# Kernel optimization log

Hardware: AMD Instinct MI355X
Metric: run time of the kernel (lower is better)

The kernel has to match this reference:

```python
import jax, jax.numpy as jnp
import numpy as np

N, CS, CZ = 512, 384, 128
H, C, PQ, PV = 12, 16, 4, 8
NB = 8
EPS = 1e-8


def _ln(x, g, b):
    m = jnp.mean(x, axis=-1, keepdims=True)
    v = jnp.mean((x - m) ** 2, axis=-1, keepdims=True)
    return (x - m) / jnp.sqrt(v + 1e-5) * g + b


def _quat_rot(bcd):
    # (1, b, c, d) quaternion -> rotation matrix, as in AF2 BackboneUpdate
    ones = jnp.ones(bcd.shape[:-1] + (1,), bcd.dtype)
    q = jnp.concatenate([ones, bcd], axis=-1)
    q = q / jnp.linalg.norm(q, axis=-1, keepdims=True)
    w, x, y, z = q[..., 0], q[..., 1], q[..., 2], q[..., 3]
    R = jnp.stack([
        1 - 2 * (y * y + z * z), 2 * (x * y - w * z), 2 * (x * z + w * y),
        2 * (x * y + w * z), 1 - 2 * (x * x + z * z), 2 * (y * z - w * x),
        2 * (x * z - w * y), 2 * (y * z + w * x), 1 - 2 * (x * x + y * y),
    ], axis=-1)
    return R.reshape(bcd.shape[:-1] + (3, 3))


def _ipa(s, z, R, t, p):
    n = s.shape[0]
    q = (s @ p['w_q']).reshape(n, H, C)
    kv = (s @ p['w_kv']).reshape(n, H, 2, C)
    k, v = kv[..., 0, :], kv[..., 1, :]

    # local points -> global frames
    q_pts = (s @ p['w_qpts']).reshape(n, H * PQ, 3)
    q_pts = jnp.einsum('nxy,npy->npx', R, q_pts) + t[:, None, :]
    q_pts = q_pts.reshape(n, H, PQ, 3)
    kv_pts = (s @ p['w_kvpts']).reshape(n, H * (PQ + PV), 3)
    kv_pts = jnp.einsum('nxy,npy->npx', R, kv_pts) + t[:, None, :]
    kv_pts = kv_pts.reshape(n, H, PQ + PV, 3)
    k_pts, v_pts = kv_pts[:, :, :PQ], kv_pts[:, :, PQ:]

    b = z @ p['w_b']  # [i, j, H]

    scalar = jnp.einsum('ihc,jhc->hij', q, k) / np.sqrt(C)
    # sum_p ||q_ip - k_jp||^2 expanded to avoid [N,N,H,P,3] intermediate
    sq_q = jnp.sum(q_pts ** 2, axis=(-1, -2)).T  # [H, i]
    sq_k = jnp.sum(k_pts ** 2, axis=(-1, -2)).T  # [H, j]
    cross = jnp.einsum('ihpc,jhpc->hij', q_pts, k_pts)
    d2 = sq_q[:, :, None] + sq_k[:, None, :] - 2.0 * cross  # [H, i, j]

    gamma = jax.nn.softplus(p['head_weights'])  # [H]
    w_C = np.sqrt(2.0 / (9.0 * PQ))
    w_L = np.sqrt(1.0 / 3.0)
    logits = w_L * (scalar + jnp.transpose(b, (2, 0, 1))
                    - gamma[:, None, None] * (w_C / 2.0) * d2)
    a = jax.nn.softmax(logits, axis=-1)  # [H, i, j]

    o = jnp.einsum('hij,jhc->ihc', a, v).reshape(n, H * C)
    o_pt = jnp.einsum('hij,jhpc->ihpc', a, v_pts)
    # back to local frame: R_i^{-1} (o_pt - t_i)
    o_pt = jnp.einsum('nyx,nhpy->nhpx', R, o_pt - t[:, None, None, :])
    o_pt_norm = jnp.sqrt(jnp.sum(o_pt ** 2, axis=-1) + EPS)  # [n, H, PV]
    o_pair = jnp.einsum('hij,ijz->ihz', a, z).reshape(n, H * CZ)

    cat = jnp.concatenate([o, o_pt.reshape(n, H * PV * 3),
                           o_pt_norm.reshape(n, H * PV), o_pair], axis=-1)
    return cat @ p['w_out'] + p['b_out']


def _forward(s, z, p):
    n = s.shape[0]
    R = jnp.broadcast_to(jnp.eye(3, dtype=s.dtype), (n, 3, 3))
    t = jnp.zeros((n, 3), s.dtype)
    for _ in range(NB):  # shared weights across blocks, as in AF2
        s = s + _ipa(s, z, R, t, p)
        s = _ln(s, p['ln1_g'], p['ln1_b'])
        h = jax.nn.relu(s @ p['w_t1'])
        h = jax.nn.relu(h @ p['w_t2'])
        s = s + h @ p['w_t3']
        s = _ln(s, p['ln2_g'], p['ln2_b'])
        upd = s @ p['w_bb'] + p['b_bb']  # [n, 6]
        Ru = _quat_rot(upd[:, :3])
        tu = upd[:, 3:]
        t = jnp.einsum('nxy,ny->nx', R, tu) + t
        R = jnp.einsum('nxy,nyz->nxz', R, Ru)
    return jnp.concatenate([s, t], axis=-1)  # [n, CS + 3]


def setup_inputs() -> dict:
    key = jax.random.key(0)
    ks = jax.random.split(key, 12)
    sc = 0.02
    cat_dim = H * C + H * PV * 3 + H * PV + H * CZ  # 2112
    return {
        's': jax.random.normal(ks[0], (N, CS), jnp.float32),
        'z': jax.random.normal(ks[1], (N, N, CZ), jnp.float32),
        'w_q': jax.random.normal(ks[2], (CS, H * C), jnp.float32) * sc,
        'w_kv': jax.random.normal(ks[3], (CS, H * 2 * C), jnp.float32) * sc,
        'w_qpts': jax.random.normal(ks[4], (CS, H * PQ * 3), jnp.float32) * sc,
        'w_kvpts': jax.random.normal(ks[5], (CS, H * (PQ + PV) * 3), jnp.float32) * sc,
        'w_b': jax.random.normal(ks[6], (CZ, H), jnp.float32) * sc,
        'head_weights': jnp.zeros((H,), jnp.float32),
        'w_out': jax.random.normal(ks[7], (cat_dim, CS), jnp.float32) * sc,
        'b_out': jnp.zeros((CS,), jnp.float32),
        'ln1_g': jnp.ones((CS,), jnp.float32),
        'ln1_b': jnp.zeros((CS,), jnp.float32),
        'w_t1': jax.random.normal(ks[8], (CS, CS), jnp.float32) * sc,
        'w_t2': jax.random.normal(ks[9], (CS, CS), jnp.float32) * sc,
        'w_t3': jax.random.normal(ks[10], (CS, CS), jnp.float32) * sc,
        'ln2_g': jnp.ones((CS,), jnp.float32),
        'ln2_b': jnp.zeros((CS,), jnp.float32),
        'w_bb': jax.random.normal(ks[11], (CS, 6), jnp.float32) * sc,
        'b_bb': jnp.zeros((6,), jnp.float32),
    }


def reference(s, z, w_q, w_kv, w_qpts, w_kvpts, w_b, head_weights, w_out,
              b_out, ln1_g, ln1_b, w_t1, w_t2, w_t3, ln2_g, ln2_b, w_bb, b_bb):
    p = dict(w_q=w_q, w_kv=w_kv, w_qpts=w_qpts, w_kvpts=w_kvpts, w_b=w_b,
             head_weights=head_weights, w_out=w_out, b_out=b_out,
             ln1_g=ln1_g, ln1_b=ln1_b, w_t1=w_t1, w_t2=w_t2, w_t3=w_t3,
             ln2_g=ln2_g, ln2_b=ln2_b, w_bb=w_bb, b_bb=b_bb)
    return _forward(s, z, p)
```

## Files before the change

kernel.cpp:

```cpp
#include <hip/hip_runtime.h>
#include <hip/hip_bf16.h>

constexpr int Nres = 512;
constexpr int Cs   = 384;
constexpr int Cz   = 128;
constexpr int NH   = 12;
constexpr int HC   = 16;
constexpr int NPQ  = 4;
constexpr int NPV  = 8;
constexpr int NBLK = 8;
constexpr int PROJD = NH*HC + NH*2*HC + NH*NPQ*3 + NH*(NPQ+NPV)*3;
constexpr int CATD = NH*HC + NH*NPV*3 + NH*NPV + NH*Cz;
constexpr float W_L  = 0.57735026918962576f;
constexpr float W_C2 = 0.11785113019775793f;

using u16 = unsigned short;
typedef __bf16 bf16x8 __attribute__((ext_vector_type(8)));
typedef float  f32x4  __attribute__((ext_vector_type(4)));

static inline int gdiv(int n, int b) { return (n + b - 1) / b; }

static __device__ __forceinline__ u16 f2bf(float x) {
    __hip_bfloat16 h = __float2bfloat16(x);
    return *reinterpret_cast<u16*>(&h);
}
static __device__ __forceinline__ float bf2f(u16 x) {
    return __bfloat162float(*reinterpret_cast<__hip_bfloat16*>(&x));
}

__global__ void k_init(const float* __restrict__ s_in, float* __restrict__ s_cur,
                       u16* __restrict__ s_bf,
                       float* __restrict__ R, float* __restrict__ t) {
    int idx = blockIdx.x * blockDim.x + threadIdx.x;
    if (idx < Nres * Cs) { float v = s_in[idx]; s_cur[idx] = v; s_bf[idx] = f2bf(v); }
    if (idx < Nres * 9) {
        int e = idx % 9;
        R[idx] = (e == 0 || e == 4 || e == 8) ? 1.f : 0.f;
    }
    if (idx < Nres * 3) t[idx] = 0.f;
}

__global__ void k_concatW(const float* __restrict__ w_q, const float* __restrict__ w_kv,
                          const float* __restrict__ w_qpts, const float* __restrict__ w_kvpts,
                          float* __restrict__ Wcat) {
    int idx = blockIdx.x * blockDim.x + threadIdx.x;
    if (idx >= Cs * PROJD) return;
    int k = idx / PROJD, n = idx - k * PROJD;
    float v;
    if      (n < 192) v = w_q[k * 192 + n];
    else if (n < 576) v = w_kv[k * 384 + (n - 192)];
    else if (n < 720) v = w_qpts[k * 144 + (n - 576)];
    else              v = w_kvpts[k * 432 + (n - 720)];
    Wcat[idx] = v;
}

__global__ void k_transposeW(const float* __restrict__ in, u16* __restrict__ out,
                             int K, int N) {
    __shared__ float tile[32][33];
    int n0 = blockIdx.x * 32, k0 = blockIdx.y * 32;
    int tx = threadIdx.x & 31, ty = threadIdx.x >> 5;
#pragma unroll
    for (int j = 0; j < 4; j++)
        tile[ty + j * 8][tx] = in[(size_t)(k0 + ty + j * 8) * N + n0 + tx];
    __syncthreads();
#pragma unroll
    for (int j = 0; j < 4; j++)
        out[(size_t)(n0 + ty + j * 8) * K + k0 + tx] = f2bf(tile[tx][ty + j * 8]);
}

__global__ void k_zT(const float* __restrict__ z, u16* __restrict__ zT) {
    __shared__ float tile[32][33];
    int i  = blockIdx.x;
    int j0 = blockIdx.y * 32;
    int c0 = blockIdx.z * 32;
    int tx = threadIdx.x & 31, ty = threadIdx.x >> 5;
    const float* src = z + (size_t)i * Nres * Cz;
#pragma unroll
    for (int l = 0; l < 4; l++)
        tile[ty + l * 8][tx] = src[(size_t)(j0 + ty + l * 8) * Cz + c0 + tx];
    __syncthreads();
    u16* dst = zT + (size_t)i * Cz * Nres;
#pragma unroll
    for (int l = 0; l < 4; l++)
        dst[(size_t)(c0 + ty + l * 8) * Nres + j0 + tx] = f2bf(tile[tx][ty + l * 8]);
}

__global__ void __launch_bounds__(256)
k_gemm_mfma(const u16* __restrict__ A, const u16* __restrict__ Bt,
            float* __restrict__ P, int M, int K, int N, int Kc) {
    __shared__ u16 As[2][64 * 40];
    __shared__ u16 Bs[2][64 * 40];
    const int tid = threadIdx.x;
    const int m0 = blockIdx.y * 64;
    const int n0 = blockIdx.x * 64;
    const int kbeg = blockIdx.z * Kc;
    const int kend = kbeg + Kc;
    const int wv = tid >> 6, lane = tid & 63;
    const int wm = (wv >> 1) * 32, wn = (wv & 1) * 32;
    const int lrow = lane & 15, lq = lane >> 4;

    f32x4 zero = {0.f, 0.f, 0.f, 0.f};
    f32x4 acc00 = zero, acc01 = zero, acc10 = zero, acc11 = zero;

    const int srow = tid >> 2;
    const int sko  = (tid & 3) * 8;
    const size_t aoff = (size_t)(m0 + srow) * K + sko;
    const size_t boff = (size_t)(n0 + srow) * K + sko;

    uint4 ra = *(const uint4*)&A[aoff + kbeg];
    uint4 rb = *(const uint4*)&Bt[boff + kbeg];
    *(uint4*)&As[0][srow * 40 + sko] = ra;
    *(uint4*)&Bs[0][srow * 40 + sko] = rb;
    __syncthreads();

    int buf = 0;
    for (int k0 = kbeg; k0 < kend; k0 += 32) {
        const bool nxt = (k0 + 32 < kend);
        if (nxt) {
            ra = *(const uint4*)&A[aoff + k0 + 32];
            rb = *(const uint4*)&Bt[boff + k0 + 32];
        }
        bf16x8 a0 = *reinterpret_cast<const bf16x8*>(&As[buf][(wm + lrow) * 40 + lq * 8]);
        bf16x8 a1 = *reinterpret_cast<const bf16x8*>(&As[buf][(wm + 16 + lrow) * 40 + lq * 8]);
        bf16x8 b0 = *reinterpret_cast<const bf16x8*>(&Bs[buf][(wn + lrow) * 40 + lq * 8]);
        bf16x8 b1 = *reinterpret_cast<const bf16x8*>(&Bs[buf][(wn + 16 + lrow) * 40 + lq * 8]);
        acc00 = __builtin_amdgcn_mfma_f32_16x16x32_bf16(a0, b0, acc00, 0, 0, 0);
        acc01 = __builtin_amdgcn_mfma_f32_16x16x32_bf16(a0, b1, acc01, 0, 0, 0);
        acc10 = __builtin_amdgcn_mfma_f32_16x16x32_bf16(a1, b0, acc10, 0, 0, 0);
        acc11 = __builtin_amdgcn_mfma_f32_16x16x32_bf16(a1, b1, acc11, 0, 0, 0);
        if (nxt) {
            *(uint4*)&As[buf ^ 1][srow * 40 + sko] = ra;
            *(uint4*)&Bs[buf ^ 1][srow * 40 + sko] = rb;
            __syncthreads();
            buf ^= 1;
        }
    }
    float* Pp = P + (size_t)blockIdx.z * M * N;
    const int rbase = m0 + wm + lq * 4;
    const int cbase = n0 + wn + lrow;
#pragma unroll
    for (int r = 0; r < 4; r++) {
        Pp[(size_t)(rbase + r) * N + cbase]           = acc00[r];
        Pp[(size_t)(rbase + r) * N + cbase + 16]      = acc01[r];
        Pp[(size_t)(rbase + 16 + r) * N + cbase]      = acc10[r];
        Pp[(size_t)(rbase + 16 + r) * N + cbase + 16] = acc11[r];
    }
}

__global__ void __launch_bounds__(256)
k_gemm_rbf(const u16* __restrict__ A, const u16* __restrict__ Bt,
           float* __restrict__ outf, u16* __restrict__ outb,
           int M, int K, int N, int relu_bf) {
    __shared__ u16 As[2][32 * 40];
    __shared__ u16 Bs[2][64 * 40];
    const int tid = threadIdx.x;
    const int m0 = blockIdx.y * 32;
    const int n0 = blockIdx.x * 64;
    const int wv = tid >> 6, lane = tid & 63;
    const int wm = (wv >> 1) * 16, wn = (wv & 1) * 32;
    const int lrow = lane & 15, lq = lane >> 4;
    f32x4 zero = {0.f, 0.f, 0.f, 0.f};
    f32x4 acc0 = zero, acc1 = zero;
    const int srow = tid >> 2, sko = (tid & 3) * 8;
    const size_t aoff = (size_t)(m0 + srow) * K + sko;
    const size_t boff = (size_t)(n0 + srow) * K + sko;

    uint4 ra, rb;
    if (tid < 128) ra = *(const uint4*)&A[aoff];
    rb = *(const uint4*)&Bt[boff];
    if (tid < 128) *(uint4*)&As[0][srow * 40 + sko] = ra;
    *(uint4*)&Bs[0][srow * 40 + sko] = rb;
    __syncthreads();

    int buf = 0;
    for (int k0 = 0; k0 < K; k0 += 32) {
        const bool nxt = (k0 + 32 < K);
        if (nxt) {
            if (tid < 128) ra = *(const uint4*)&A[aoff + k0 + 32];
            rb = *(const uint4*)&Bt[boff + k0 + 32];
        }
        bf16x8 a  = *reinterpret_cast<const bf16x8*>(&As[buf][(wm + lrow) * 40 + lq * 8]);
        bf16x8 b0 = *reinterpret_cast<const bf16x8*>(&Bs[buf][(wn + lrow) * 40 + lq * 8]);
        bf16x8 b1 = *reinterpret_cast<const bf16x8*>(&Bs[buf][(wn + 16 + lrow) * 40 + lq * 8]);
        acc0 = __builtin_amdgcn_mfma_f32_16x16x32_bf16(a, b0, acc0, 0, 0, 0);
        acc1 = __builtin_amdgcn_mfma_f32_16x16x32_bf16(a, b1, acc1, 0, 0, 0);
        if (nxt) {
            if (tid < 128) *(uint4*)&As[buf ^ 1][srow * 40 + sko] = ra;
            *(uint4*)&Bs[buf ^ 1][srow * 40 + sko] = rb;
            __syncthreads();
            buf ^= 1;
        }
    }
    const int rbase = m0 + wm + lq * 4;
    const int cbase = n0 + wn + lrow;
    if (relu_bf) {
#pragma unroll
        for (int r = 0; r < 4; r++) {
            outb[(size_t)(rbase + r) * N + cbase]      = f2bf(fmaxf(acc0[r], 0.f));
            outb[(size_t)(rbase + r) * N + cbase + 16] = f2bf(fmaxf(acc1[r], 0.f));
        }
    } else {
#pragma unroll
        for (int r = 0; r < 4; r++) {
            outf[(size_t)(rbase + r) * N + cbase]      = acc0[r];
            outf[(size_t)(rbase + r) * N + cbase + 16] = acc1[r];
        }
    }
}

__global__ void k_bproj(const float* __restrict__ z, const float* __restrict__ w_b,
                        float* __restrict__ b_hij) {
    __shared__ float zs[16][129];
    __shared__ float wbs[Cz * NH];
    const int tid = threadIdx.x;
    const int base = blockIdx.x * 16;
#pragma unroll
    for (int l = 0; l < 6; l++) {
        int idx = tid + l * 256;
        if (idx < Cz * NH) wbs[idx] = w_b[idx];
    }
#pragma unroll
    for (int l = 0; l < 8; l++) {
        int idx = tid + l * 256;
        int r = idx >> 7, c = idx & 127;
        zs[r][c] = z[(size_t)(base + r) * Cz + c];
    }
    __syncthreads();
    if (tid < 192) {
        int h = tid >> 4, r = tid & 15;
        float acc = 0.f;
        for (int c = 0; c < Cz; c++) acc += zs[r][c] * wbs[c * NH + h];
        int row = base + r;
        int i = row >> 9, j = row & 511;
        b_hij[((size_t)h * Nres + i) * Nres + j] = acc * W_L;
    }
}

__global__ void k_prep(const float* __restrict__ proj, const float* __restrict__ R,
                       const float* __restrict__ t, const float* __restrict__ hw,
                       u16* __restrict__ Aaug, u16* __restrict__ Baug,
                       u16* __restrict__ vhT) {
    int idx = blockIdx.x * blockDim.x + threadIdx.x;
    if (idx >= NH * Nres) return;
    int h = idx / Nres, i = idx % Nres;
    float R_[9], t_[3];
#pragma unroll
    for (int e = 0; e < 9; e++) R_[e] = R[i * 9 + e];
#pragma unroll
    for (int e = 0; e < 3; e++) t_[e] = t[i * 3 + e];
    const float* prow = proj + (size_t)i * PROJD;
    float gam = log1pf(__expf(hw[h]));
    float ch  = sqrtf(2.f * gam * W_C2);

    u16 arow[32], brow[32];
#pragma unroll
    for (int c = 0; c < HC; c++) {
        arow[c] = f2bf(prow[h * HC + c] * (W_L * 0.25f));
        brow[c] = f2bf(prow[192 + h * 2 * HC + c]);
        vhT[((size_t)h * 48 + c) * Nres + i] = f2bf(prow[192 + h * 2 * HC + HC + c]);
    }
#pragma unroll
    for (int p = 0; p < NPQ; p++) {
        const float* src = prow + 576 + (h * NPQ + p) * 3;
        float y0 = src[0], y1 = src[1], y2 = src[2];
        float v0 = R_[0]*y0 + R_[1]*y1 + R_[2]*y2 + t_[0];
        float v1 = R_[3]*y0 + R_[4]*y1 + R_[5]*y2 + t_[1];
        float v2 = R_[6]*y0 + R_[7]*y1 + R_[8]*y2 + t_[2];
        float s = W_L * ch;
        arow[16 + p*3 + 0] = f2bf(v0 * s);
        arow[16 + p*3 + 1] = f2bf(v1 * s);
        arow[16 + p*3 + 2] = f2bf(v2 * s);
    }
    float sk = 0.f;
#pragma unroll
    for (int p = 0; p < NPQ + NPV; p++) {
        const float* src = prow + 720 + (h * (NPQ+NPV) + p) * 3;
        float y0 = src[0], y1 = src[1], y2 = src[2];
        float v0 = R_[0]*y0 + R_[1]*y1 + R_[2]*y2 + t_[0];
        float v1 = R_[3]*y0 + R_[4]*y1 + R_[5]*y2 + t_[1];
        float v2 = R_[6]*y0 + R_[7]*y1 + R_[8]*y2 + t_[2];
        if (p < NPQ) {
            brow[16 + p*3 + 0] = f2bf(v0 * ch);
            brow[16 + p*3 + 1] = f2bf(v1 * ch);
            brow[16 + p*3 + 2] = f2bf(v2 * ch);
            sk += v0*v0 + v1*v1 + v2*v2;
        } else {
            int c0 = 16 + (p - NPQ) * 3;
            vhT[((size_t)h * 48 + c0 + 0) * Nres + i] = f2bf(v0);
            vhT[((size_t)h * 48 + c0 + 1) * Nres + i] = f2bf(v1);
            vhT[((size_t)h * 48 + c0 + 2) * Nres + i] = f2bf(v2);
        }
    }
    float x = -W_L * gam * W_C2 * sk;
    u16 hi = f2bf(x);
    float lo = x - bf2f(hi);
    arow[28] = f2bf(1.0f); arow[29] = f2bf(1.0f); arow[30] = 0; arow[31] = 0;
    brow[28] = hi;         brow[29] = f2bf(lo);   brow[30] = 0; brow[31] = 0;

    uint4* ad = (uint4*)&Aaug[((size_t)h * Nres + i) * 32];
    uint4* bd = (uint4*)&Baug[((size_t)h * Nres + i) * 32];
    const uint4* as = (const uint4*)arow;
    const uint4* bs = (const uint4*)brow;
#pragma unroll
    for (int e = 0; e < 4; e++) { ad[e] = as[e]; bd[e] = bs[e]; }
}

__global__ void __launch_bounds__(256)
k_attn(const u16* __restrict__ Aaug, const u16* __restrict__ Baug,
       const float* __restrict__ b_hij, const u16* __restrict__ vhT,
       const float* __restrict__ R, const float* __restrict__ t,
       u16* __restrict__ Pbf, u16* __restrict__ cat_bf) {
    __shared__ union {
        struct { u16 A[64 * 40]; u16 B[512 * 40]; } qk;
        u16 P[64 * 520];
    } U;
    __shared__ u16 Bsv[2][48 * 40];
    __shared__ float Ct[64 * 49];

    const int i0 = blockIdx.x * 64;
    const int h  = blockIdx.y;
    const int tid = threadIdx.x;
    const int wv = tid >> 6, lane = tid & 63;
    const int lrow = lane & 15, lq = lane >> 4;
    const int wm = wv * 16;
    const int srow = tid >> 2, sko = (tid & 3) * 8;

    const u16* Bp = vhT + (size_t)h * 48 * Nres;
    const size_t boff = (size_t)srow * Nres + sko;
    if (tid < 192) {
        uint4 rv = *(const uint4*)&Bp[boff];
        *(uint4*)&Bsv[0][srow * 40 + sko] = rv;
    }

    {
        int r4 = tid >> 2, q = tid & 3;
        *(uint4*)&U.qk.A[r4 * 40 + q * 8] =
            *(const uint4*)&Aaug[((size_t)h * Nres + i0 + r4) * 32 + q * 8];
#pragma unroll
        for (int l = 0; l < 8; l++) {
            int idx = tid + l * 256;
            int rr = idx >> 2, qq = idx & 3;
            *(uint4*)&U.qk.B[rr * 40 + qq * 8] =
                *(const uint4*)&Baug[((size_t)h * Nres + rr) * 32 + qq * 8];
        }
    }
    __syncthreads();

    f32x4 zero = {0.f, 0.f, 0.f, 0.f};
    bf16x8 afrag = *reinterpret_cast<const bf16x8*>(&U.qk.A[(wm + lrow) * 40 + lq * 8]);
    f32x4 acc[32];
#pragma unroll
    for (int tt = 0; tt < 32; tt++) {
        bf16x8 bfr = *reinterpret_cast<const bf16x8*>(&U.qk.B[(tt * 16 + lrow) * 40 + lq * 8]);
        acc[tt] = __builtin_amdgcn_mfma_f32_16x16x32_bf16(afrag, bfr, zero, 0, 0, 0);
    }
    const float* bh = b_hij + ((size_t)h * Nres + (i0 + wm + lq * 4)) * Nres;
#pragma unroll
    for (int tt = 0; tt < 32; tt++) {
#pragma unroll
        for (int r = 0; r < 4; r++)
            acc[tt][r] += bh[(size_t)r * Nres + tt * 16 + lrow];
    }
    float mx[4] = {-1e30f, -1e30f, -1e30f, -1e30f};
#pragma unroll
    for (int tt = 0; tt < 32; tt++)
#pragma unroll
        for (int r = 0; r < 4; r++) mx[r] = fmaxf(mx[r], acc[tt][r]);
#pragma unroll
    for (int off = 8; off > 0; off >>= 1)
#pragma unroll
        for (int r = 0; r < 4; r++) mx[r] = fmaxf(mx[r], __shfl_xor(mx[r], off));
    float sm[4] = {0.f, 0.f, 0.f, 0.f};
#pragma unroll
    for (int tt = 0; tt < 32; tt++)
#pragma unroll
        for (int r = 0; r < 4; r++) { acc[tt][r] = __expf(acc[tt][r] - mx[r]); sm[r] += acc[tt][r]; }
#pragma unroll
    for (int off = 8; off > 0; off >>= 1)
#pragma unroll
        for (int r = 0; r < 4; r++) sm[r] += __shfl_xor(sm[r], off);
    float inv[4];
#pragma unroll
    for (int r = 0; r < 4; r++) inv[r] = 1.f / sm[r];

    __syncthreads();

#pragma unroll
    for (int tt = 0; tt < 32; tt++)
#pragma unroll
        for (int r = 0; r < 4; r++)
            U.P[(wm + lq * 4 + r) * 520 + tt * 16 + lrow] = f2bf(acc[tt][r] * inv[r]);
    __syncthreads();

#pragma unroll
    for (int l = 0; l < 16; l++) {
        int v = tid + l * 256;
        int rr = v >> 6, cq = v & 63;
        *(uint4*)&Pbf[((size_t)h * Nres + i0 + rr) * 512 + cq * 8] =
            *(const uint4*)&U.P[rr * 520 + cq * 8];
    }

    f32x4 o0 = zero, o1 = zero, o2 = zero;
    int buf = 0;
    for (int k0 = 0; k0 < Nres; k0 += 32) {
        const bool nxt = (k0 + 32 < Nres);
        uint4 rv;
        if (nxt && tid < 192) rv = *(const uint4*)&Bp[boff + k0 + 32];
        bf16x8 a  = *reinterpret_cast<const bf16x8*>(&U.P[(wm + lrow) * 520 + k0 + lq * 8]);
        bf16x8 b0 = *reinterpret_cast<const bf16x8*>(&Bsv[buf][(lrow) * 40 + lq * 8]);
        bf16x8 b1 = *reinterpret_cast<const bf16x8*>(&Bsv[buf][(16 + lrow) * 40 + lq * 8]);
        bf16x8 b2 = *reinterpret_cast<const bf16x8*>(&Bsv[buf][(32 + lrow) * 40 + lq * 8]);
        o0 = __builtin_amdgcn_mfma_f32_16x16x32_bf16(a, b0, o0, 0, 0, 0);
        o1 = __builtin_amdgcn_mfma_f32_16x16x32_bf16(a, b1, o1, 0, 0, 0);
        o2 = __builtin_amdgcn_mfma_f32_16x16x32_bf16(a, b2, o2, 0, 0, 0);
        if (nxt) {
            if (tid < 192) *(uint4*)&Bsv[buf ^ 1][srow * 40 + sko] = rv;
            __syncthreads();
            buf ^= 1;
        }
    }
#pragma unroll
    for (int r = 0; r < 4; r++) {
        int row = wm + lq * 4 + r;
        Ct[row * 49 + lrow]      = o0[r];
        Ct[row * 49 + 16 + lrow] = o1[r];
        Ct[row * 49 + 32 + lrow] = o2[r];
    }
    __syncthreads();
#pragma unroll
    for (int l = 0; l < 4; l++) {
        int idx = tid + l * 256;
        int r = idx >> 4, c = idx & 15;
        cat_bf[(size_t)(i0 + r) * CATD + h * HC + c] = f2bf(Ct[r * 49 + c]);
    }
#pragma unroll
    for (int l = 0; l < 2; l++) {
        int idx = tid + l * 256;
        int r = idx >> 3, p = idx & 7;
        int i = i0 + r;
        float g0 = Ct[r * 49 + 16 + p * 3 + 0];
        float g1 = Ct[r * 49 + 16 + p * 3 + 1];
        float g2 = Ct[r * 49 + 16 + p * 3 + 2];
        float d0 = g0 - t[i * 3 + 0], d1 = g1 - t[i * 3 + 1], d2v = g2 - t[i * 3 + 2];
        const float* Rn = R + i * 9;
        float l0 = Rn[0] * d0 + Rn[3] * d1 + Rn[6] * d2v;
        float l1 = Rn[1] * d0 + Rn[4] * d1 + Rn[7] * d2v;
        float l2 = Rn[2] * d0 + Rn[5] * d1 + Rn[8] * d2v;
        int hp = h * NPV + p;
        u16* crow = cat_bf + (size_t)i * CATD;
        crow[192 + hp * 3 + 0] = f2bf(l0);
        crow[192 + hp * 3 + 1] = f2bf(l1);
        crow[192 + hp * 3 + 2] = f2bf(l2);
        crow[480 + hp] = f2bf(sqrtf(l0 * l0 + l1 * l1 + l2 * l2 + 1e-8f));
    }
}

__global__ void __launch_bounds__(256)
k_opair(const u16* __restrict__ Pbf, const u16* __restrict__ zT,
        u16* __restrict__ cat_bf) {
    __shared__ u16 P_lds[16 * 520];
    __shared__ u16 Bs[2][128 * 40];
    const int i = blockIdx.x;
    const int tid = threadIdx.x;
    const int wv = tid >> 6, ln = tid & 63;
    const int srow = tid >> 2, sko = (tid & 3) * 8;
    const u16* Bp = zT + (size_t)i * Cz * Nres;
    const size_t b0off = (size_t)srow * Nres + sko;
    const size_t b1off = (size_t)(64 + srow) * Nres + sko;

    uint4 rb0 = *(const uint4*)&Bp[b0off];
    uint4 rb1 = *(const uint4*)&Bp[b1off];

#pragma unroll
    for (int l = 0; l < 3; l++) {
        int v = tid + l * 256;
        int hh = v >> 6, cq = v & 63;
        *(uint4*)&P_lds[hh * 520 + cq * 8] =
            *(const uint4*)&Pbf[((size_t)hh * Nres + i) * 512 + cq * 8];
    }
    for (int l = tid; l < 4 * 520; l += 256) P_lds[12 * 520 + l] = 0;

    *(uint4*)&Bs[0][srow * 40 + sko]        = rb0;
    *(uint4*)&Bs[0][(64 + srow) * 40 + sko] = rb1;
    __syncthreads();

    const int lrow = ln & 15, lq = ln >> 4;
    const int wn = wv * 32;
    f32x4 zero = {0.f, 0.f, 0.f, 0.f};
    f32x4 acc0 = zero, acc1 = zero;
    int buf = 0;
    for (int k0 = 0; k0 < Nres; k0 += 32) {
        const bool nxt = (k0 + 32 < Nres);
        if (nxt) {
            rb0 = *(const uint4*)&Bp[b0off + k0 + 32];
            rb1 = *(const uint4*)&Bp[b1off + k0 + 32];
        }
        bf16x8 a  = *reinterpret_cast<const bf16x8*>(&P_lds[lrow * 520 + k0 + lq * 8]);
        bf16x8 b0 = *reinterpret_cast<const bf16x8*>(&Bs[buf][(wn + lrow) * 40 + lq * 8]);
        bf16x8 b1 = *reinterpret_cast<const bf16x8*>(&Bs[buf][(wn + 16 + lrow) * 40 + lq * 8]);
        acc0 = __builtin_amdgcn_mfma_f32_16x16x32_bf16(a, b0, acc0, 0, 0, 0);
        acc1 = __builtin_amdgcn_mfma_f32_16x16x32_bf16(a, b1, acc1, 0, 0, 0);
        if (nxt) {
            *(uint4*)&Bs[buf ^ 1][srow * 40 + sko]        = rb0;
            *(uint4*)&Bs[buf ^ 1][(64 + srow) * 40 + sko] = rb1;
            __syncthreads();
            buf ^= 1;
        }
    }
    u16* crow = cat_bf + (size_t)i * CATD + 576;
#pragma unroll
    for (int r = 0; r < 4; r++) {
        int row = lq * 4 + r;
        if (row < NH) {
            crow[row * Cz + wn + lrow]      = f2bf(acc0[r]);
            crow[row * Cz + wn + 16 + lrow] = f2bf(acc1[r]);
        }
    }
}

__global__ void k_reduce_ln(const float* __restrict__ P, const float* __restrict__ bias,
                            float* __restrict__ s, u16* __restrict__ s_bf,
                            const float* __restrict__ g, const float* __restrict__ b,
                            int nsplit) {
    __shared__ float red[512];
    int i = blockIdx.x, tid = threadIdx.x;
    float v = s[(size_t)i * Cs + tid];
    if (bias) v += bias[tid];
    for (int sp = 0; sp < nsplit; sp++) v += P[(size_t)sp * Nres * Cs + (size_t)i * Cs + tid];
    red[tid] = v;
    if (tid < 128) red[384 + tid] = 0.f;
    __syncthreads();
    for (int st = 256; st > 0; st >>= 1) { if (tid < st) red[tid] += red[tid + st]; __syncthreads(); }
    float mean = red[0] / Cs;
    __syncthreads();
    float d = v - mean;
    red[tid] = d * d;
    if (tid < 128) red[384 + tid] = 0.f;
    __syncthreads();
    for (int st = 256; st > 0; st >>= 1) { if (tid < st) red[tid] += red[tid + st]; __syncthreads(); }
    float var = red[0] / Cs;
    float o = d * rsqrtf(var + 1e-5f) * g[tid] + b[tid];
    s[(size_t)i * Cs + tid] = o;
    s_bf[(size_t)i * Cs + tid] = f2bf(o);
}

__global__ void k_reduce_ln_bb(const float* __restrict__ P, float* __restrict__ s,
                               u16* __restrict__ s_bf,
                               const float* __restrict__ g, const float* __restrict__ b,
                               int nsplit,
                               const float* __restrict__ w_bb, const float* __restrict__ b_bb,
                               float* __restrict__ R, float* __restrict__ t) {
    __shared__ float red[512];
    __shared__ float uw[36];
    int i = blockIdx.x, tid = threadIdx.x;
    float v = s[(size_t)i * Cs + tid];
    for (int sp = 0; sp < nsplit; sp++) v += P[(size_t)sp * Nres * Cs + (size_t)i * Cs + tid];
    red[tid] = v;
    if (tid < 128) red[384 + tid] = 0.f;
    __syncthreads();
    for (int st = 256; st > 0; st >>= 1) { if (tid < st) red[tid] += red[tid + st]; __syncthreads(); }
    float mean = red[0] / Cs;
    __syncthreads();
    float d = v - mean;
    red[tid] = d * d;
    if (tid < 128) red[384 + tid] = 0.f;
    __syncthreads();
    for (int st = 256; st > 0; st >>= 1) { if (tid < st) red[tid] += red[tid + st]; __syncthreads(); }
    float var = red[0] / Cs;
    float o = d * rsqrtf(var + 1e-5f) * g[tid] + b[tid];
    s[(size_t)i * Cs + tid] = o;
    s_bf[(size_t)i * Cs + tid] = f2bf(o);

    float u[6];
#pragma unroll
    for (int dd = 0; dd < 6; dd++) u[dd] = o * w_bb[tid * 6 + dd];
#pragma unroll
    for (int off = 32; off > 0; off >>= 1)
#pragma unroll
        for (int dd = 0; dd < 6; dd++) u[dd] += __shfl_xor(u[dd], off);
    int wv = tid >> 6, lane = tid & 63;
    if (lane == 0) {
#pragma unroll
        for (int dd = 0; dd < 6; dd++) uw[wv * 6 + dd] = u[dd];
    }
    __syncthreads();
    if (tid == 0) {
        float uu[6];
#pragma unroll
        for (int dd = 0; dd < 6; dd++) {
            float a = b_bb[dd];
            for (int w = 0; w < 6; w++) a += uw[w * 6 + dd];
            uu[dd] = a;
        }
        float qb = uu[0], qc = uu[1], qd = uu[2];
        float inv = rsqrtf(1.f + qb*qb + qc*qc + qd*qd);
        float w = inv, x = qb * inv, y = qc * inv, zq = qd * inv;
        float Ru[9] = {
            1.f - 2.f*(y*y + zq*zq), 2.f*(x*y - w*zq),       2.f*(x*zq + w*y),
            2.f*(x*y + w*zq),        1.f - 2.f*(x*x + zq*zq), 2.f*(y*zq - w*x),
            2.f*(x*zq - w*y),        2.f*(y*zq + w*x),        1.f - 2.f*(x*x + y*y)
        };
        float Ro[9];
#pragma unroll
        for (int e = 0; e < 9; e++) Ro[e] = R[i * 9 + e];
        float tu0 = uu[3], tu1 = uu[4], tu2 = uu[5];
        t[i*3+0] += Ro[0]*tu0 + Ro[1]*tu1 + Ro[2]*tu2;
        t[i*3+1] += Ro[3]*tu0 + Ro[4]*tu1 + Ro[5]*tu2;
        t[i*3+2] += Ro[6]*tu0 + Ro[7]*tu1 + Ro[8]*tu2;
#pragma unroll
        for (int r = 0; r < 3; r++)
#pragma unroll
            for (int c = 0; c < 3; c++)
                R[i*9 + r*3 + c] = Ro[r*3+0]*Ru[0*3+c] + Ro[r*3+1]*Ru[1*3+c] + Ro[r*3+2]*Ru[2*3+c];
    }
}

__global__ void k_final(const float* __restrict__ s, const float* __restrict__ t,
                        float* __restrict__ out) {
    int idx = blockIdx.x * blockDim.x + threadIdx.x;
    if (idx >= Nres * (Cs + 3)) return;
    int i = idx / (Cs + 3), c = idx - i * (Cs + 3);
    out[idx] = (c < Cs) ? s[(size_t)i * Cs + c] : t[i * 3 + (c - Cs)];
}

extern "C" void kernel_launch(void* const* d_in, const int* in_sizes, int n_in,
                              void* d_out, int out_size, void* d_ws, size_t ws_size,
                              hipStream_t stream) {
    const float* s_in    = (const float*)d_in[0];
    const float* z       = (const float*)d_in[1];
    const float* w_q     = (const float*)d_in[2];
    const float* w_kv    = (const float*)d_in[3];
    const float* w_qpts  = (const float*)d_in[4];
    const float* w_kvpts = (const float*)d_in[5];
    const float* w_b     = (const float*)d_in[6];
    const float* hw      = (const float*)d_in[7];
    const float* w_out   = (const float*)d_in[8];
    const float* b_out   = (const float*)d_in[9];
    const float* ln1_g   = (const float*)d_in[10];
    const float* ln1_b   = (const float*)d_in[11];
    const float* w_t1    = (const float*)d_in[12];
    const float* w_t2    = (const float*)d_in[13];
    const float* w_t3    = (const float*)d_in[14];
    const float* ln2_g   = (const float*)d_in[15];
    const float* ln2_b   = (const float*)d_in[16];
    const float* w_bb    = (const float*)d_in[17];
    const float* b_bb    = (const float*)d_in[18];
    float* out = (float*)d_out;

    float* ws = (float*)d_ws;
    size_t off = 0;
    float* s_cur = ws + off; off += (size_t)Nres * Cs;
    float* b_hij = ws + off; off += (size_t)NH * Nres * Nres;
    float* proj  = ws + off; off += (size_t)Nres * PROJD;
    float* Wcat  = ws + off; off += (size_t)Cs * PROJD;
    float* Rbuf  = ws + off; off += (size_t)Nres * 9;
    float* tbuf  = ws + off; off += (size_t)Nres * 3;
    float* Pslab = ws + off; off += (size_t)11 * Nres * Cs;
    u16* s_bf   = (u16*)(ws + off); off += (size_t)Nres * Cs / 2;
    u16* cat_bf = (u16*)(ws + off); off += (size_t)Nres * CATD / 2;
    u16* h1_bf  = (u16*)(ws + off); off += (size_t)Nres * Cs / 2;
    u16* h2_bf  = (u16*)(ws + off); off += (size_t)Nres * Cs / 2;
    u16* WcatT  = (u16*)(ws + off); off += (size_t)Cs * PROJD / 2;
    u16* w_outT = (u16*)(ws + off); off += (size_t)CATD * Cs / 2;
    u16* w_t1T  = (u16*)(ws + off); off += (size_t)Cs * Cs / 2;
    u16* w_t2T  = (u16*)(ws + off); off += (size_t)Cs * Cs / 2;
    u16* w_t3T  = (u16*)(ws + off); off += (size_t)Cs * Cs / 2;
    u16* Pbf    = (u16*)(ws + off); off += (size_t)NH * Nres * Nres / 2;
    u16* vhTbf  = (u16*)(ws + off); off += (size_t)NH * 48 * Nres / 2;
    u16* Aaug   = (u16*)(ws + off); off += (size_t)NH * Nres * 32 / 2;
    u16* Baug   = (u16*)(ws + off); off += (size_t)NH * Nres * 32 / 2;
    u16* zTbf   = (u16*)(ws + off); off += (size_t)Nres * Cz * Nres / 2;

    k_init<<<gdiv(Nres*Cs, 256), 256, 0, stream>>>(s_in, s_cur, s_bf, Rbuf, tbuf);
    k_concatW<<<gdiv(Cs*PROJD, 256), 256, 0, stream>>>(w_q, w_kv, w_qpts, w_kvpts, Wcat);
    k_transposeW<<<dim3(PROJD/32, Cs/32), 256, 0, stream>>>(Wcat, WcatT, Cs, PROJD);
    k_transposeW<<<dim3(Cs/32, CATD/32), 256, 0, stream>>>(w_out, w_outT, CATD, Cs);
    k_transposeW<<<dim3(Cs/32, Cs/32), 256, 0, stream>>>(w_t1, w_t1T, Cs, Cs);
    k_transposeW<<<dim3(Cs/32, Cs/32), 256, 0, stream>>>(w_t2, w_t2T, Cs, Cs);
    k_transposeW<<<dim3(Cs/32, Cs/32), 256, 0, stream>>>(w_t3, w_t3T, Cs, Cs);
    k_bproj<<<Nres*Nres/16, 256, 0, stream>>>(z, w_b, b_hij);
    k_zT<<<dim3(Nres, Nres/32, Cz/32), 256, 0, stream>>>(z, zTbf);

    for (int it = 0; it < NBLK; it++) {
        k_gemm_rbf<<<dim3(PROJD/64, Nres/32), 256, 0, stream>>>(s_bf, WcatT, proj, nullptr, Nres, Cs, PROJD, 0);
        k_prep<<<gdiv(NH*Nres, 256), 256, 0, stream>>>(proj, Rbuf, tbuf, hw, Aaug, Baug, vhTbf);
        k_attn<<<dim3(Nres/64, NH), 256, 0, stream>>>(Aaug, Baug, b_hij, vhTbf, Rbuf, tbuf, Pbf, cat_bf);
        k_opair<<<Nres, 256, 0, stream>>>(Pbf, zTbf, cat_bf);
        k_gemm_mfma<<<dim3(Cs/64, Nres/64, 6), 256, 0, stream>>>(cat_bf, w_outT, Pslab, Nres, CATD, Cs, 352);
        k_reduce_ln<<<Nres, Cs, 0, stream>>>(Pslab, b_out, s_cur, s_bf, ln1_g, ln1_b, 6);
        k_gemm_rbf<<<dim3(Cs/64, Nres/32), 256, 0, stream>>>(s_bf, w_t1T, nullptr, h1_bf, Nres, Cs, Cs, 1);
        k_gemm_rbf<<<dim3(Cs/64, Nres/32), 256, 0, stream>>>(h1_bf, w_t2T, nullptr, h2_bf, Nres, Cs, Cs, 1);
        k_gemm_rbf<<<dim3(Cs/64, Nres/32), 256, 0, stream>>>(h2_bf, w_t3T, Pslab, nullptr, Nres, Cs, Cs, 0);
        k_reduce_ln_bb<<<Nres, Cs, 0, stream>>>(Pslab, s_cur, s_bf, ln2_g, ln2_b, 1, w_bb, b_bb, Rbuf, tbuf);
    }

    k_final<<<gdiv(Nres*(Cs+3), 256), 256, 0, stream>>>(s_cur, tbuf, out);
}
```

Measured before the change: 919.5 us.

## Store pair bias in bf16, transpose proj output, split-K transition GEMMs

```diff
diff --git a/kernel.cpp b/kernel.cpp
--- a/kernel.cpp
+++ b/kernel.cpp
@@ -148,9 +148,8 @@
 }
 
 __global__ void __launch_bounds__(256)
-k_gemm_rbf(const u16* __restrict__ A, const u16* __restrict__ Bt,
-           float* __restrict__ outf, u16* __restrict__ outb,
-           int M, int K, int N, int relu_bf) {
+k_gemm_proj(const u16* __restrict__ A, const u16* __restrict__ Bt,
+            float* __restrict__ outT, int M, int K, int N) {
     __shared__ u16 As[2][32 * 40];
     __shared__ u16 Bs[2][64 * 40];
     const int tid = threadIdx.x;
@@ -193,23 +192,86 @@
     }
     const int rbase = m0 + wm + lq * 4;
     const int cbase = n0 + wn + lrow;
-    if (relu_bf) {
-#pragma unroll
-        for (int r = 0; r < 4; r++) {
-            outb[(size_t)(rbase + r) * N + cbase]      = f2bf(fmaxf(acc0[r], 0.f));
-            outb[(size_t)(rbase + r) * N + cbase + 16] = f2bf(fmaxf(acc1[r], 0.f));
-        }
-    } else {
-#pragma unroll
-        for (int r = 0; r < 4; r++) {
-            outf[(size_t)(rbase + r) * N + cbase]      = acc0[r];
-            outf[(size_t)(rbase + r) * N + cbase + 16] = acc1[r];
-        }
+    *reinterpret_cast<f32x4*>(&outT[(size_t)cbase * M + rbase])        = acc0;
+    *reinterpret_cast<f32x4*>(&outT[(size_t)(cbase + 16) * M + rbase]) = acc1;
+}
+
+__global__ void __launch_bounds__(256)
+k_gemm_tr(const u16* __restrict__ Abf, const float* __restrict__ As0,
+          const float* __restrict__ As1, const u16* __restrict__ Bt,
+          float* __restrict__ Pout, int amode) {
+    __shared__ u16 Asm[2][32 * 40];
+    __shared__ u16 Bsm[2][64 * 40];
+    const int tid = threadIdx.x;
+    const int m0 = blockIdx.y * 32;
+    const int n0 = blockIdx.x * 64;
+    const int kbeg = blockIdx.z * 192;
+    const int kend = kbeg + 192;
+    const int wv = tid >> 6, lane = tid & 63;
+    const int wm = (wv >> 1) * 16, wn = (wv & 1) * 32;
+    const int lrow = lane & 15, lq = lane >> 4;
+    f32x4 zero = {0.f, 0.f, 0.f, 0.f};
+    f32x4 acc0 = zero, acc1 = zero;
+    const int srow = tid >> 2, sko = (tid & 3) * 8;
+    const int rowR = tid >> 3, c4 = (tid & 7) * 4;
+    const size_t aoffb = (size_t)(m0 + srow) * Cs + sko;
+    const size_t aoffr = (size_t)(m0 + rowR) * Cs + c4;
+    const size_t boff  = (size_t)(n0 + srow) * Cs + sko;
+
+    uint4 ra, rb;
+    float4 f0, f1;
+    rb = *(const uint4*)&Bt[boff + kbeg];
+    if (amode == 0) { if (tid < 128) ra = *(const uint4*)&Abf[aoffb + kbeg]; }
+    else { f0 = *(const float4*)&As0[aoffr + kbeg]; f1 = *(const float4*)&As1[aoffr + kbeg]; }
+
+    if (amode == 0) { if (tid < 128) *(uint4*)&Asm[0][srow * 40 + sko] = ra; }
+    else {
+        uint2 wp;
+        wp.x = (unsigned)f2bf(fmaxf(f0.x + f1.x, 0.f)) | ((unsigned)f2bf(fmaxf(f0.y + f1.y, 0.f)) << 16);
+        wp.y = (unsigned)f2bf(fmaxf(f0.z + f1.z, 0.f)) | ((unsigned)f2bf(fmaxf(f0.w + f1.w, 0.f)) << 16);
+        *(uint2*)&Asm[0][rowR * 40 + c4] = wp;
+    }
+    *(uint4*)&Bsm[0][srow * 40 + sko] = rb;
+    __syncthreads();
+
+    int buf = 0;
+    for (int k0 = kbeg; k0 < kend; k0 += 32) {
+        const bool nxt = (k0 + 32 < kend);
+        if (nxt) {
+            rb = *(const uint4*)&Bt[boff + k0 + 32];
+            if (amode == 0) { if (tid < 128) ra = *(const uint4*)&Abf[aoffb + k0 + 32]; }
+            else { f0 = *(const float4*)&As0[aoffr + k0 + 32]; f1 = *(const float4*)&As1[aoffr + k0 + 32]; }
+        }
+        bf16x8 a  = *reinterpret_cast<const bf16x8*>(&Asm[buf][(wm + lrow) * 40 + lq * 8]);
+        bf16x8 b0 = *reinterpret_cast<const bf16x8*>(&Bsm[buf][(wn + lrow) * 40 + lq * 8]);
+        bf16x8 b1 = *reinterpret_cast<const bf16x8*>(&Bsm[buf][(wn + 16 + lrow) * 40 + lq * 8]);
+        acc0 = __builtin_amdgcn_mfma_f32_16x16x32_bf16(a, b0, acc0, 0, 0, 0);
+        acc1 = __builtin_amdgcn_mfma_f32_16x16x32_bf16(a, b1, acc1, 0, 0, 0);
+        if (nxt) {
+            if (amode == 0) { if (tid < 128) *(uint4*)&Asm[buf ^ 1][srow * 40 + sko] = ra; }
+            else {
+                uint2 wp;
+                wp.x = (unsigned)f2bf(fmaxf(f0.x + f1.x, 0.f)) | ((unsigned)f2bf(fmaxf(f0.y + f1.y, 0.f)) << 16);
+                wp.y = (unsigned)f2bf(fmaxf(f0.z + f1.z, 0.f)) | ((unsigned)f2bf(fmaxf(f0.w + f1.w, 0.f)) << 16);
+                *(uint2*)&Asm[buf ^ 1][rowR * 40 + c4] = wp;
+            }
+            *(uint4*)&Bsm[buf ^ 1][srow * 40 + sko] = rb;
+            __syncthreads();
+            buf ^= 1;
+        }
+    }
+    float* Pp = Pout + (size_t)blockIdx.z * Nres * Cs;
+    const int rbase = m0 + wm + lq * 4;
+    const int cbase = n0 + wn + lrow;
+#pragma unroll
+    for (int r = 0; r < 4; r++) {
+        Pp[(size_t)(rbase + r) * Cs + cbase]      = acc0[r];
+        Pp[(size_t)(rbase + r) * Cs + cbase + 16] = acc1[r];
     }
 }
 
 __global__ void k_bproj(const float* __restrict__ z, const float* __restrict__ w_b,
-                        float* __restrict__ b_hij) {
+                        u16* __restrict__ b_hij_bf) {
     __shared__ float zs[16][129];
     __shared__ float wbs[Cz * NH];
     const int tid = threadIdx.x;
@@ -232,37 +294,37 @@
         for (int c = 0; c < Cz; c++) acc += zs[r][c] * wbs[c * NH + h];
         int row = base + r;
         int i = row >> 9, j = row & 511;
-        b_hij[((size_t)h * Nres + i) * Nres + j] = acc * W_L;
-    }
-}
-
-__global__ void k_prep(const float* __restrict__ proj, const float* __restrict__ R,
+        b_hij_bf[((size_t)h * Nres + i) * Nres + j] = f2bf(acc * W_L);
+    }
+}
+
+__global__ void k_prep(const float* __restrict__ projT, const float* __restrict__ R,
                        const float* __restrict__ t, const float* __restrict__ hw,
                        u16* __restrict__ Aaug, u16* __restrict__ Baug,
                        u16* __restrict__ vhT) {
     int idx = blockIdx.x * blockDim.x + threadIdx.x;
     if (idx >= NH * Nres) return;
     int h = idx / Nres, i = idx % Nres;
+#define PR(col) projT[(size_t)(col) * Nres + i]
     float R_[9], t_[3];
 #pragma unroll
     for (int e = 0; e < 9; e++) R_[e] = R[i * 9 + e];
 #pragma unroll
     for (int e = 0; e < 3; e++) t_[e] = t[i * 3 + e];
-    const float* prow = proj + (size_t)i * PROJD;
     float gam = log1pf(__expf(hw[h]));
     float ch  = sqrtf(2.f * gam * W_C2);
 
     u16 arow[32], brow[32];
 #pragma unroll
     for (int c = 0; c < HC; c++) {
-        arow[c] = f2bf(prow[h * HC + c] * (W_L * 0.25f));
-        brow[c] = f2bf(prow[192 + h * 2 * HC + c]);
-        vhT[((size_t)h * 48 + c) * Nres + i] = f2bf(prow[192 + h * 2 * HC + HC + c]);
+        arow[c] = f2bf(PR(h * HC + c) * (W_L * 0.25f));
+        brow[c] = f2bf(PR(192 + h * 2 * HC + c));
+        vhT[((size_t)h * 48 + c) * Nres + i] = f2bf(PR(192 + h * 2 * HC + HC + c));
     }
 #pragma unroll
     for (int p = 0; p < NPQ; p++) {
-        const float* src = prow + 576 + (h * NPQ + p) * 3;
-        float y0 = src[0], y1 = src[1], y2 = src[2];
+        int c0 = 576 + (h * NPQ + p) * 3;
+        float y0 = PR(c0 + 0), y1 = PR(c0 + 1), y2 = PR(c0 + 2);
         float v0 = R_[0]*y0 + R_[1]*y1 + R_[2]*y2 + t_[0];
         float v1 = R_[3]*y0 + R_[4]*y1 + R_[5]*y2 + t_[1];
         float v2 = R_[6]*y0 + R_[7]*y1 + R_[8]*y2 + t_[2];
@@ -274,8 +336,8 @@
     float sk = 0.f;
 #pragma unroll
     for (int p = 0; p < NPQ + NPV; p++) {
-        const float* src = prow + 720 + (h * (NPQ+NPV) + p) * 3;
-        float y0 = src[0], y1 = src[1], y2 = src[2];
+        int c0 = 720 + (h * (NPQ+NPV) + p) * 3;
+        float y0 = PR(c0 + 0), y1 = PR(c0 + 1), y2 = PR(c0 + 2);
         float v0 = R_[0]*y0 + R_[1]*y1 + R_[2]*y2 + t_[0];
         float v1 = R_[3]*y0 + R_[4]*y1 + R_[5]*y2 + t_[1];
         float v2 = R_[6]*y0 + R_[7]*y1 + R_[8]*y2 + t_[2];
@@ -285,12 +347,13 @@
             brow[16 + p*3 + 2] = f2bf(v2 * ch);
             sk += v0*v0 + v1*v1 + v2*v2;
         } else {
-            int c0 = 16 + (p - NPQ) * 3;
-            vhT[((size_t)h * 48 + c0 + 0) * Nres + i] = f2bf(v0);
-            vhT[((size_t)h * 48 + c0 + 1) * Nres + i] = f2bf(v1);
-            vhT[((size_t)h * 48 + c0 + 2) * Nres + i] = f2bf(v2);
-        }
-    }
+            int cc = 16 + (p - NPQ) * 3;
+            vhT[((size_t)h * 48 + cc + 0) * Nres + i] = f2bf(v0);
+            vhT[((size_t)h * 48 + cc + 1) * Nres + i] = f2bf(v1);
+            vhT[((size_t)h * 48 + cc + 2) * Nres + i] = f2bf(v2);
+        }
+    }
+#undef PR
     float x = -W_L * gam * W_C2 * sk;
     u16 hi = f2bf(x);
     float lo = x - bf2f(hi);
@@ -307,7 +370,7 @@
 
 __global__ void __launch_bounds__(256)
 k_attn(const u16* __restrict__ Aaug, const u16* __restrict__ Baug,
-       const float* __restrict__ b_hij, const u16* __restrict__ vhT,
+       const u16* __restrict__ b_hij_bf, const u16* __restrict__ vhT,
        const float* __restrict__ R, const float* __restrict__ t,
        u16* __restrict__ Pbf, u16* __restrict__ cat_bf) {
     __shared__ union {
@@ -354,13 +417,27 @@
         bf16x8 bfr = *reinterpret_cast<const bf16x8*>(&U.qk.B[(tt * 16 + lrow) * 40 + lq * 8]);
         acc[tt] = __builtin_amdgcn_mfma_f32_16x16x32_bf16(afrag, bfr, zero, 0, 0, 0);
     }
-    const float* bh = b_hij + ((size_t)h * Nres + (i0 + wm + lq * 4)) * Nres;
+    __syncthreads();
+
+    {
+        const u16* bhp = b_hij_bf + ((size_t)h * Nres + i0) * Nres;
+#pragma unroll
+        for (int l = 0; l < 16; l++) {
+            int v = tid + l * 256;
+            int rr = v >> 6, cq = v & 63;
+            *(uint4*)&U.P[rr * 520 + cq * 8] =
+                *(const uint4*)&bhp[(size_t)rr * Nres + cq * 8];
+        }
+    }
+    __syncthreads();
+
 #pragma unroll
     for (int tt = 0; tt < 32; tt++) {
 #pragma unroll
         for (int r = 0; r < 4; r++)
-            acc[tt][r] += bh[(size_t)r * Nres + tt * 16 + lrow];
-    }
+            acc[tt][r] += bf2f(U.P[(wm + lq * 4 + r) * 520 + tt * 16 + lrow]);
+    }
+
     float mx[4] = {-1e30f, -1e30f, -1e30f, -1e30f};
 #pragma unroll
     for (int tt = 0; tt < 32; tt++)
@@ -650,16 +727,14 @@
     float* ws = (float*)d_ws;
     size_t off = 0;
     float* s_cur = ws + off; off += (size_t)Nres * Cs;
-    float* b_hij = ws + off; off += (size_t)NH * Nres * Nres;
-    float* proj  = ws + off; off += (size_t)Nres * PROJD;
+    float* projT = ws + off; off += (size_t)Nres * PROJD;
     float* Wcat  = ws + off; off += (size_t)Cs * PROJD;
     float* Rbuf  = ws + off; off += (size_t)Nres * 9;
     float* tbuf  = ws + off; off += (size_t)Nres * 3;
     float* Pslab = ws + off; off += (size_t)11 * Nres * Cs;
+    u16* b_hij_bf = (u16*)(ws + off); off += (size_t)NH * Nres * Nres / 2;
     u16* s_bf   = (u16*)(ws + off); off += (size_t)Nres * Cs / 2;
     u16* cat_bf = (u16*)(ws + off); off += (size_t)Nres * CATD / 2;
-    u16* h1_bf  = (u16*)(ws + off); off += (size_t)Nres * Cs / 2;
-    u16* h2_bf  = (u16*)(ws + off); off += (size_t)Nres * Cs / 2;
     u16* WcatT  = (u16*)(ws + off); off += (size_t)Cs * PROJD / 2;
     u16* w_outT = (u16*)(ws + off); off += (size_t)CATD * Cs / 2;
     u16* w_t1T  = (u16*)(ws + off); off += (size_t)Cs * Cs / 2;
@@ -671,6 +746,8 @@
     u16* Baug   = (u16*)(ws + off); off += (size_t)NH * Nres * 32 / 2;
     u16* zTbf   = (u16*)(ws + off); off += (size_t)Nres * Cz * Nres / 2;
 
+    const int MNs = Nres * Cs;
+
     k_init<<<gdiv(Nres*Cs, 256), 256, 0, stream>>>(s_in, s_cur, s_bf, Rbuf, tbuf);
     k_concatW<<<gdiv(Cs*PROJD, 256), 256, 0, stream>>>(w_q, w_kv, w_qpts, w_kvpts, Wcat);
     k_transposeW<<<dim3(PROJD/32, Cs/32), 256, 0, stream>>>(Wcat, WcatT, Cs, PROJD);
@@ -678,20 +755,20 @@
     k_transposeW<<<dim3(Cs/32, Cs/32), 256, 0, stream>>>(w_t1, w_t1T, Cs, Cs);
     k_transposeW<<<dim3(Cs/32, Cs/32), 256, 0, stream>>>(w_t2, w_t2T, Cs, Cs);
     k_transposeW<<<dim3(Cs/32, Cs/32), 256, 0, stream>>>(w_t3, w_t3T, Cs, Cs);
-    k_bproj<<<Nres*Nres/16, 256, 0, stream>>>(z, w_b, b_hij);
+    k_bproj<<<Nres*Nres/16, 256, 0, stream>>>(z, w_b, b_hij_bf);
     k_zT<<<dim3(Nres, Nres/32, Cz/32), 256, 0, stream>>>(z, zTbf);
 
     for (int it = 0; it < NBLK; it++) {
-        k_gemm_rbf<<<dim3(PROJD/64, Nres/32), 256, 0, stream>>>(s_bf, WcatT, proj, nullptr, Nres, Cs, PROJD, 0);
-        k_prep<<<gdiv(NH*Nres, 256), 256, 0, stream>>>(proj, Rbuf, tbuf, hw, Aaug, Baug, vhTbf);
-        k_attn<<<dim3(Nres/64, NH), 256, 0, stream>>>(Aaug, Baug, b_hij, vhTbf, Rbuf, tbuf, Pbf, cat_bf);
+        k_gemm_proj<<<dim3(PROJD/64, Nres/32), 256, 0, stream>>>(s_bf, WcatT, projT, Nres, Cs, PROJD);
+        k_prep<<<gdiv(NH*Nres, 256), 256, 0, stream>>>(projT, Rbuf, tbuf, hw, Aaug, Baug, vhTbf);
+        k_attn<<<dim3(Nres/64, NH), 256, 0, stream>>>(Aaug, Baug, b_hij_bf, vhTbf, Rbuf, tbuf, Pbf, cat_bf);
         k_opair<<<Nres, 256, 0, stream>>>(Pbf, zTbf, cat_bf);
         k_gemm_mfma<<<dim3(Cs/64, Nres/64, 6), 256, 0, stream>>>(cat_bf, w_outT, Pslab, Nres, CATD, Cs, 352);
         k_reduce_ln<<<Nres, Cs, 0, stream>>>(Pslab, b_out, s_cur, s_bf, ln1_g, ln1_b, 6);
-        k_gemm_rbf<<<dim3(Cs/64, Nres/32), 256, 0, stream>>>(s_bf, w_t1T, nullptr, h1_bf, Nres, Cs, Cs, 1);
-        k_gemm_rbf<<<dim3(Cs/64, Nres/32), 256, 0, stream>>>(h1_bf, w_t2T, nullptr, h2_bf, Nres, Cs, Cs, 1);
-        k_gemm_rbf<<<dim3(Cs/64, Nres/32), 256, 0, stream>>>(h2_bf, w_t3T, Pslab, nullptr, Nres, Cs, Cs, 0);
-        k_reduce_ln_bb<<<Nres, Cs, 0, stream>>>(Pslab, s_cur, s_bf, ln2_g, ln2_b, 1, w_bb, b_bb, Rbuf, tbuf);
+        k_gemm_tr<<<dim3(Cs/64, Nres/32, 2), 256, 0, stream>>>(s_bf, nullptr, nullptr, w_t1T, Pslab, 0);
+        k_gemm_tr<<<dim3(Cs/64, Nres/32, 2), 256, 0, stream>>>(nullptr, Pslab, Pslab + MNs, w_t2T, Pslab + 2*MNs, 1);
+        k_gemm_tr<<<dim3(Cs/64, Nres/32, 2), 256, 0, stream>>>(nullptr, Pslab + 2*MNs, Pslab + 3*MNs, w_t3T, Pslab + 4*MNs, 1);
+        k_reduce_ln_bb<<<Nres, Cs, 0, stream>>>(Pslab + 4*MNs, s_cur, s_bf, ln2_g, ln2_b, 2, w_bb, b_bb, Rbuf, tbuf);
     }
 
     k_final<<<gdiv(Nres*(Cs+3), 256), 256, 0, stream>>>(s_cur, tbuf, out);
```

Result: faster. 896.1 us (-2.5%).
